# Optimization experiments

Measured on AMD Instinct MI355X. Metric: run time of the kernel, lower is better.

Reference implementation:

```python
import jax, jax.numpy as jnp
import numpy as np

MAX_RADIUS = 1.5
NUM_BASIS = 10
CS, CV = 16, 4              # scalar / vector multiplicities (input = query = key = output irreps)
DIM = CS + 3 * CV           # 28
SILU_GAIN = 1.679           # e3nn normalize2mom gain for silu


def _sus(x):
    # e3nn soft_unit_step: exp(-1/x) for x>0 else 0
    xp = jnp.where(x > 0, x, 1.0)
    return jnp.where(x > 0, jnp.exp(-1.0 / xp), 0.0)


def _fc(emb, w1, w2):
    # FullyConnectedNet([NUM_BASIS, 16, numel], act=silu), fan-in normalized
    h = SILU_GAIN * jax.nn.silu(emb @ w1 / jnp.sqrt(float(NUM_BASIS)))
    return h @ w2 / jnp.sqrt(16.0)


def _tp(fs, fv, sh1, w):
    # FullyConnectedTensorProduct((CS x0e + CV x1o) x (1x0e + 1x1o)) with per-edge weights w [...,400]
    # paths: 0e*0e->0e, 0e*1o->1o, 1o*0e->1o, 1o*1o->0e (sh l=0 component == 1)
    i0 = CS * CS; i1 = i0 + CS * CV; i2 = i1 + CV * CV
    lead = w.shape[:-1]
    w1 = w[..., :i0].reshape(lead + (CS, CS))
    w2 = w[..., i0:i1].reshape(lead + (CS, CV))
    w3 = w[..., i1:i2].reshape(lead + (CV, CV))
    w4 = w[..., i2:].reshape(lead + (CV, CS))
    out_s = (jnp.einsum('...c,...co->...o', fs, w1) / jnp.sqrt(float(CS))
             + jnp.einsum('...cx,...x,...co->...o', fv, sh1, w4) / jnp.sqrt(3.0 * CV)) / jnp.sqrt(2.0)
    out_v = (jnp.einsum('...c,...x,...co->...ox', fs, sh1, w2) / jnp.sqrt(float(CS))
             + jnp.einsum('...cx,...co->...ox', fv, w3) / jnp.sqrt(float(CV))) / jnp.sqrt(2.0)
    return out_s, out_v


def _forward(f, pos, wq_s, wq_v, fck_w1, fck_w2, fcv_w1, fcv_w2, dot_ws, dot_wv):
    B, N, _ = f.shape
    fs = f[..., :CS]                                    # [B,N,CS]
    fv = f[..., CS:].reshape(B, N, CV, 3)               # [B,N,CV,3]
    valid = jnp.any(f != 0, axis=-1)                    # mask of non-padded nodes

    # dense radius graph: i = dst, j = src; edge_vec = pos[src] - pos[dst]
    dvec = pos[:, None, :, :] - pos[:, :, None, :]      # [B,i,j,3]
    dist = jnp.sqrt(jnp.sum(dvec * dvec, axis=-1) + 1e-12)
    eye = jnp.eye(N, dtype=bool)
    mask = (dist < MAX_RADIUS) & (~eye)[None] & valid[:, :, None] & valid[:, None, :]
    sh1 = jnp.sqrt(3.0) * dvec / dist[..., None]        # component-normalized l=1 spherical harmonics

    # soft_one_hot_linspace, basis='smooth_finite', cutoff=True, scaled by sqrt(NB)
    step = MAX_RADIUS / (NUM_BASIS + 1)
    centers = jnp.linspace(0.0, MAX_RADIUS, NUM_BASIS + 2)[1:-1]
    diff = (dist[..., None] - centers) / step
    emb = (1.14136 * np.e ** 2) * _sus(diff + 1.0) * _sus(1.0 - diff)
    emb = emb * jnp.sqrt(float(NUM_BASIS))
    cutoff = _sus(10.0 * (1.0 - dist / MAX_RADIUS)) * mask

    # q = h_q(f): per-l linear
    q_s = fs @ wq_s / jnp.sqrt(float(CS))
    q_v = jnp.einsum('bncx,co->bnox', fv, wq_v) / jnp.sqrt(float(CV))

    wk = _fc(emb, fck_w1, fck_w2)                       # [B,N,N,400] per-edge TP weights
    wv = _fc(emb, fcv_w1, fcv_w2)
    k_s, k_v = _tp(fs[:, None], fv[:, None], sh1, wk)   # gather f[src] via broadcast over dst axis
    v_s, v_v = _tp(fs[:, None], fv[:, None], sh1, wv)

    # dot(q[dst], k) -> scalar per edge
    score = (jnp.einsum('bic,bijd,cd->bij', q_s, k_s, dot_ws) / jnp.sqrt(float(CS))
             + jnp.einsum('bicx,bijdx,cd->bij', q_v, k_v, dot_wv) / jnp.sqrt(3.0 * CV)) / jnp.sqrt(2.0)
    log_exp = cutoff * score
    z = jnp.sum(log_exp, axis=-1)                       # scatter-sum over src per dst node
    z = jnp.where(z == 0, 1.0, z)
    alpha = log_exp / z[:, :, None]
    r = jax.nn.relu(alpha)
    att = jnp.where(r > 0, jnp.sqrt(jnp.where(r > 0, r, 1.0)), 0.0)

    out_s = jnp.einsum('bij,bijo->bio', att, v_s)       # scatter-aggregate
    out_v = jnp.einsum('bij,bijox->biox', att, v_v)
    out = jnp.concatenate([out_s, out_v.reshape(B, N, 3 * CV)], axis=-1)
    return out * valid[..., None].astype(out.dtype)


def setup_inputs() -> dict:
    key = jax.random.key(0)
    ks = jax.random.split(key, 10)
    B, N = 4, 192
    NUMEL = CS * CS + CS * CV + CV * CV + CV * CS       # 400
    n = jax.random.normal
    return {
        'f': n(ks[0], (B, N, DIM), dtype=jnp.float32),
        'pos': 5.0 * jax.random.uniform(ks[1], (B, N, 3), dtype=jnp.float32),
        'wq_s': n(ks[2], (CS, CS), dtype=jnp.float32),
        'wq_v': n(ks[3], (CV, CV), dtype=jnp.float32),
        'fck_w1': n(ks[4], (NUM_BASIS, 16), dtype=jnp.float32),
        'fck_w2': n(ks[5], (16, NUMEL), dtype=jnp.float32),
        'fcv_w1': n(ks[6], (NUM_BASIS, 16), dtype=jnp.float32),
        'fcv_w2': n(ks[7], (16, NUMEL), dtype=jnp.float32),
        'dot_ws': n(ks[8], (CS, CS), dtype=jnp.float32),
        'dot_wv': n(ks[9], (CV, CV), dtype=jnp.float32),
    }


def reference(f, pos, wq_s, wq_v, fck_w1, fck_w2, fcv_w1, fcv_w2, dot_ws, dot_wv):
    return _forward(f, pos, wq_s, wq_v, fck_w1, fck_w2, fcv_w1, fcv_w2, dot_ws, dot_wv)
```

## Files before the change

kernel.cpp:

```cpp
#include <hip/hip_runtime.h>
#include <math.h>


#define NN 192
#define TSTRIDE 2560
#define MAXM 192

constexpr float C1   = 0.17677669529663687f;
constexpr float C2   = 0.17677669529663687f;
constexpr float C3   = 0.35355339059327373f;
constexpr float C4   = 0.20412414523193154f;
constexpr float CS1f = 0.17677669529663687f;
constexpr float CS2f = 0.20412414523193154f;
constexpr float RS10 = 0.31622776601683794f;
constexpr float GAIN4 = 1.679f * 0.25f;
constexpr float SQRT3 = 1.7320508075688772f;
constexpr float CEMB = (float)(1.14136 * 7.3890560989306495 * 3.1622776601683795);

__global__ __launch_bounds__(256) void precomp(
  const float* __restrict__ f, const float* __restrict__ wq_s, const float* __restrict__ wq_v,
  const float* __restrict__ w2k, const float* __restrict__ w2v,
  const float* __restrict__ dws, const float* __restrict__ dwv,
  float* __restrict__ T, float* __restrict__ qd, float* __restrict__ validf)
{
  const int node = blockIdx.x;
  const int tid  = threadIdx.x;
  __shared__ float Wsh[12800];
  __shared__ float fsh[28];
  __shared__ float qs_sh[16], qv_sh[12];
  __shared__ int vsh;
  if (tid == 0) vsh = 0;
  if (tid < 28) fsh[tid] = f[node*28 + tid];
  {
    float4* d = (float4*)Wsh;
    const float4* s0 = (const float4*)w2k;
    const float4* s1 = (const float4*)w2v;
    for (int q = tid; q < 1600; q += 256) { d[q] = s0[q]; d[1600 + q] = s1[q]; }
  }
  __syncthreads();
  if (tid < 28 && fsh[tid] != 0.f) vsh = 1;
  if (tid < 16) {
    float a = 0.f;
    #pragma unroll
    for (int c = 0; c < 16; ++c) a = fmaf(fsh[c], wq_s[c*16 + tid], a);
    qs_sh[tid] = a * 0.25f;
  } else if (tid < 28) {
    int idx = tid - 16, o = idx / 3, x = idx - o*3;
    float a = 0.f;
    #pragma unroll
    for (int c = 0; c < 4; ++c) a = fmaf(fsh[16 + c*3 + x], wq_v[c*4 + o], a);
    qv_sh[idx] = a * 0.5f;
  }
  __syncthreads();
  if (tid < 16) {
    float a = 0.f;
    #pragma unroll
    for (int c = 0; c < 16; ++c) a = fmaf(qs_sh[c], dws[c*16 + tid], a);
    qd[node*28 + tid] = a * CS1f;
  } else if (tid < 28) {
    int idx = tid - 16, d = idx / 3, x = idx - d*3;
    float a = 0.f;
    #pragma unroll
    for (int c = 0; c < 4; ++c) a = fmaf(qv_sh[c*3 + x], dwv[c*4 + d], a);
    qd[node*28 + tid] = a * CS2f;
  }
  if (tid == 0) validf[node] = vsh ? 1.f : 0.f;

  for (int e = tid; e < 2560; e += 256) {
    const int fc = e >= 1280 ? 1 : 0;
    const int r = e - fc*1280;
    const int h = r / 80, q = r - h*80;
    const float* W = Wsh + fc*6400 + h*400;
    float val = 0.f;
    if (q < 16) {
      #pragma unroll
      for (int c = 0; c < 16; ++c) val = fmaf(fsh[c], W[c*16 + q], val);
      val *= C1;
    } else if (q < 20) {
      const int o = q - 16;
      #pragma unroll
      for (int c = 0; c < 16; ++c) val = fmaf(fsh[c], W[256 + c*4 + o], val);
      val *= C2;
    } else if (q < 32) {
      const int p = q - 20, o = p / 3, x = p - o*3;
      #pragma unroll
      for (int c = 0; c < 4; ++c) val = fmaf(fsh[16 + c*3 + x], W[320 + c*4 + o], val);
      val *= C3;
    } else {
      const int p = q - 32, o = p / 3, x = p - o*3;
      #pragma unroll
      for (int c = 0; c < 4; ++c) val = fmaf(fsh[16 + c*3 + x], W[336 + c*16 + o], val);
      val *= C4;
    }
    T[(size_t)node*TSTRIDE + fc*1280 + (q >> 2)*64 + h*4 + (q & 3)] = val;
  }
}

__global__ __launch_bounds__(256) void se3_main(
  const float* __restrict__ pos, const float* __restrict__ w1k, const float* __restrict__ w1v,
  const float* __restrict__ T, const float* __restrict__ qd, const float* __restrict__ validf,
  float* __restrict__ out)
{
  const int bi = blockIdx.x;
  const int b = bi / NN, i = bi - b*NN;
  const int tid = threadIdx.x;
  const int lane = tid & 63, wid = tid >> 6;

  __shared__ float qd_sh[28];
  __shared__ float w1_sh[320];
  __shared__ int   s_node[MAXM];
  __shared__ float s_cut[MAXM], s_dist[MAXM];
  __shared__ float s_shx[MAXM], s_shy[MAXM], s_shz[MAXM];
  __shared__ float emb_sh[MAXM*10];
  __shared__ float Hk_sh[MAXM*16];
  __shared__ float Hv_sh[MAXM*16];
  __shared__ float le_sh[MAXM];
  __shared__ float att_sh[MAXM];
  __shared__ int   cnt_sh;
  __shared__ float red_sh[4];
  __shared__ float opart[4][28];

  if (tid < 28) qd_sh[tid] = qd[bi*28 + tid];
  if (tid < 160) {
    w1_sh[tid]       = w1k[tid] * RS10;
    w1_sh[160 + tid] = w1v[tid] * RS10;
  }
  if (tid == 0) cnt_sh = 0;
  const float pix = pos[bi*3+0], piy = pos[bi*3+1], piz = pos[bi*3+2];
  const float vali = validf[bi];
  __syncthreads();

  if (tid < NN) {
    const int nj = b*NN + tid;
    const float dx = pos[nj*3+0]-pix, dy = pos[nj*3+1]-piy, dz = pos[nj*3+2]-piz;
    const float dist = sqrtf(fmaf(dx,dx,fmaf(dy,dy,dz*dz)) + 1e-12f);
    if (tid != i && dist < 1.5f && vali != 0.f && validf[nj] != 0.f) {
      const float cut = expf(-1.f / (10.f * (1.f - dist * (1.f/1.5f))));
      if (cut > 0.f) {
        const int s = atomicAdd(&cnt_sh, 1);
        const float sc = SQRT3 / dist;
        s_node[s] = nj; s_cut[s] = cut; s_dist[s] = dist;
        s_shx[s] = dx*sc; s_shy[s] = dy*sc; s_shz[s] = dz*sc;
      }
    }
  }
  __syncthreads();
  const int M = cnt_sh;
  const int MK = M * 16;

  for (int idx = tid; idx < M*10; idx += 256) {
    const int pr = idx / 10, k = idx - pr*10;
    const float dd = (s_dist[pr] - (float)(k+1)*(1.5f/11.f)) * (11.f/1.5f);
    float e = 0.f;
    if (dd > -1.f && dd < 1.f) e = CEMB * expf(-1.f/(1.f+dd) - 1.f/(1.f-dd));
    emb_sh[idx] = e;
  }
  __syncthreads();

  for (int idx = tid; idx < M*32; idx += 256) {
    const int pr = idx >> 5, t = idx & 31, h = t & 15;
    const float* w = w1_sh + (t >> 4)*160;
    const float* e = emb_sh + pr*10;
    float s = 0.f;
    #pragma unroll
    for (int q = 0; q < 10; ++q) s = fmaf(e[q], w[q*16 + h], s);
    const float hh = GAIN4 * s / (1.f + expf(-s));
    float* dst = (t < 16) ? Hk_sh : Hv_sh;
    dst[pr*16 + h] = hh;
  }
  __syncthreads();

  for (int idx = tid; idx < MK; idx += 256) {
    const int pr = idx >> 4, h = idx & 15;
    const int node = s_node[pr];
    const float sx = s_shx[pr], sy = s_shy[pr], sz = s_shz[pr];
    const float a = Hk_sh[idx];
    const float4* b4 = (const float4*)(T + (size_t)node*TSTRIDE);
    float cc[80];
    float4* c4 = (float4*)cc;
    #pragma unroll
    for (int q = 0; q < 20; ++q) c4[q] = b4[q*16 + h];
    float s = 0.f;
    #pragma unroll
    for (int o = 0; o < 16; ++o) {
      const float t4 = fmaf(cc[32+3*o], sx, fmaf(cc[33+3*o], sy, cc[34+3*o]*sz));
      s = fmaf(qd_sh[o], cc[o] + t4, s);
    }
    #pragma unroll
    for (int o = 0; o < 4; ++o) {
      const float qvs = fmaf(qd_sh[16+3*o], sx, fmaf(qd_sh[17+3*o], sy, qd_sh[18+3*o]*sz));
      s = fmaf(qvs, cc[16+o], s);
      s = fmaf(qd_sh[16+3*o], cc[20+3*o+0], s);
      s = fmaf(qd_sh[17+3*o], cc[20+3*o+1], s);
      s = fmaf(qd_sh[18+3*o], cc[20+3*o+2], s);
    }
    s *= a;
    #pragma unroll
    for (int d = 1; d < 16; d <<= 1) s += __shfl_xor(s, d);
    if ((tid & 15) == 0) le_sh[pr] = s;
  }
  __syncthreads();

  float les = 0.f;
  if (tid < M) les = s_cut[tid] * le_sh[tid];
  float z = les;
  #pragma unroll
  for (int d = 1; d < 64; d <<= 1) z += __shfl_xor(z, d);
  if (lane == 0) red_sh[wid] = z;
  __syncthreads();
  z = red_sh[0] + red_sh[1] + red_sh[2] + red_sh[3];
  if (z == 0.f) z = 1.f;
  if (tid < M) {
    const float alpha = les / z;
    att_sh[tid] = alpha > 0.f ? sqrtf(alpha) : 0.f;
  }
  __syncthreads();

  float acc[28];
  #pragma unroll
  for (int c = 0; c < 28; ++c) acc[c] = 0.f;
  for (int idx = tid; idx < MK; idx += 256) {
    const int pr = idx >> 4, h = idx & 15;
    const int node = s_node[pr];
    const float sx = s_shx[pr], sy = s_shy[pr], sz = s_shz[pr];
    const float a = Hv_sh[idx] * att_sh[pr];
    const float4* b4 = (const float4*)(T + (size_t)node*TSTRIDE + 1280);
    float cc[80];
    float4* c4 = (float4*)cc;
    #pragma unroll
    for (int q = 0; q < 20; ++q) c4[q] = b4[q*16 + h];
    #pragma unroll
    for (int o = 0; o < 16; ++o) {
      const float t4 = fmaf(cc[32+3*o], sx, fmaf(cc[33+3*o], sy, cc[34+3*o]*sz));
      acc[o] = fmaf(a, cc[o] + t4, acc[o]);
    }
    const float ax = a*sx, ay = a*sy, az = a*sz;
    #pragma unroll
    for (int o = 0; o < 4; ++o) {
      const float t2 = cc[16+o];
      acc[16+3*o+0] = fmaf(ax, t2, fmaf(a, cc[20+3*o+0], acc[16+3*o+0]));
      acc[16+3*o+1] = fmaf(ay, t2, fmaf(a, cc[20+3*o+1], acc[16+3*o+1]));
      acc[16+3*o+2] = fmaf(az, t2, fmaf(a, cc[20+3*o+2], acc[16+3*o+2]));
    }
  }

  #pragma unroll
  for (int c = 0; c < 28; ++c) {
    float w = acc[c];
    #pragma unroll
    for (int d = 1; d < 64; d <<= 1) w += __shfl_xor(w, d);
    if (lane == 0) opart[wid][c] = w;
  }
  __syncthreads();
  if (tid < 28) out[bi*28 + tid] = opart[0][tid] + opart[1][tid] + opart[2][tid] + opart[3][tid];
}

extern "C" void kernel_launch(void* const* d_in, const int* in_sizes, int n_in,
                              void* d_out, int out_size, void* d_ws, size_t ws_size,
                              hipStream_t stream) {
  const float* f      = (const float*)d_in[0];
  const float* pos    = (const float*)d_in[1];
  const float* wq_s   = (const float*)d_in[2];
  const float* wq_v   = (const float*)d_in[3];
  const float* fck_w1 = (const float*)d_in[4];
  const float* fck_w2 = (const float*)d_in[5];
  const float* fcv_w1 = (const float*)d_in[6];
  const float* fcv_w2 = (const float*)d_in[7];
  const float* dot_ws = (const float*)d_in[8];
  const float* dot_wv = (const float*)d_in[9];
  float* outp = (float*)d_out;

  const int BN = in_sizes[0] / 28;

  float* T   = (float*)d_ws;
  float* qdp = T + (size_t)BN * TSTRIDE;
  float* vf  = qdp + (size_t)BN * 28;

  precomp<<<BN, 256, 0, stream>>>(f, wq_s, wq_v, fck_w2, fcv_w2, dot_ws, dot_wv, T, qdp, vf);
  se3_main<<<BN, 256, 0, stream>>>(pos, fck_w1, fcv_w1, T, qdp, vf, outp);
}
```

Measured before the change: 102.8 us.

## Fuse attention normalization into single pass using sign-split deferred sqrt accumulators

Merges the embedding, radial MLP, key-score, softmax-like normalization and value accumulation into one loop over neighbor×channel items. The attention weight sqrt(le/z) is rewritten as sqrt(le)/sqrt(z). Separate accumulators for positive and negative le are kept, and the sign of z picks one of them at the end. This removes several block barriers, the LDS staging arrays and a second pass over the neighbors. In exchange, each thread recomputes the radial basis and MLP for its item, and the doubled register accumulators raise register pressure.

After: 136.2 us. 1.32x slower.

```diff
diff --git a/kernel.cpp b/kernel.cpp
--- a/kernel.cpp
+++ b/kernel.cpp
@@ -111,14 +111,8 @@
   __shared__ int   s_node[MAXM];
   __shared__ float s_cut[MAXM], s_dist[MAXM];
   __shared__ float s_shx[MAXM], s_shy[MAXM], s_shz[MAXM];
-  __shared__ float emb_sh[MAXM*10];
-  __shared__ float Hk_sh[MAXM*16];
-  __shared__ float Hv_sh[MAXM*16];
-  __shared__ float le_sh[MAXM];
-  __shared__ float att_sh[MAXM];
   __shared__ int   cnt_sh;
-  __shared__ float red_sh[4];
-  __shared__ float opart[4][28];
+  __shared__ float opart[4][57];
 
   if (tid < 28) qd_sh[tid] = qd[bi*28 + tid];
   if (tid < 160) {
@@ -148,38 +142,40 @@
   const int M = cnt_sh;
   const int MK = M * 16;
 
-  for (int idx = tid; idx < M*10; idx += 256) {
-    const int pr = idx / 10, k = idx - pr*10;
-    const float dd = (s_dist[pr] - (float)(k+1)*(1.5f/11.f)) * (11.f/1.5f);
-    float e = 0.f;
-    if (dd > -1.f && dd < 1.f) e = CEMB * expf(-1.f/(1.f+dd) - 1.f/(1.f-dd));
-    emb_sh[idx] = e;
-  }
-  __syncthreads();
-
-  for (int idx = tid; idx < M*32; idx += 256) {
-    const int pr = idx >> 5, t = idx & 31, h = t & 15;
-    const float* w = w1_sh + (t >> 4)*160;
-    const float* e = emb_sh + pr*10;
-    float s = 0.f;
-    #pragma unroll
-    for (int q = 0; q < 10; ++q) s = fmaf(e[q], w[q*16 + h], s);
-    const float hh = GAIN4 * s / (1.f + expf(-s));
-    float* dst = (t < 16) ? Hk_sh : Hv_sh;
-    dst[pr*16 + h] = hh;
-  }
-  __syncthreads();
+  float accP[28], accN[28];
+  #pragma unroll
+  for (int c = 0; c < 28; ++c) { accP[c] = 0.f; accN[c] = 0.f; }
+  float zacc = 0.f;
 
   for (int idx = tid; idx < MK; idx += 256) {
     const int pr = idx >> 4, h = idx & 15;
     const int node = s_node[pr];
+    const float dist = s_dist[pr], cut = s_cut[pr];
     const float sx = s_shx[pr], sy = s_shy[pr], sz = s_shz[pr];
-    const float a = Hk_sh[idx];
-    const float4* b4 = (const float4*)(T + (size_t)node*TSTRIDE);
+
+    float emb[10];
+    #pragma unroll
+    for (int k = 0; k < 10; ++k) {
+      const float dd = (dist - (float)(k+1)*(1.5f/11.f)) * (11.f/1.5f);
+      float e = 0.f;
+      if (dd > -1.f && dd < 1.f) e = CEMB * expf(-1.f/(1.f+dd) - 1.f/(1.f-dd));
+      emb[k] = e;
+    }
+    float sk = 0.f, sv = 0.f;
+    #pragma unroll
+    for (int q = 0; q < 10; ++q) {
+      sk = fmaf(emb[q], w1_sh[q*16 + h], sk);
+      sv = fmaf(emb[q], w1_sh[160 + q*16 + h], sv);
+    }
+    const float Hk = GAIN4 * sk / (1.f + expf(-sk));
+    const float Hv = GAIN4 * sv / (1.f + expf(-sv));
+
+    const float4* __restrict__ bk = (const float4*)(T + (size_t)node*TSTRIDE);
     float cc[80];
     float4* c4 = (float4*)cc;
-    #pragma unroll
-    for (int q = 0; q < 20; ++q) c4[q] = b4[q*16 + h];
+
+    #pragma unroll
+    for (int q = 0; q < 20; ++q) c4[q] = bk[q*16 + h];
     float s = 0.f;
     #pragma unroll
     for (int o = 0; o < 16; ++o) {
@@ -194,65 +190,68 @@
       s = fmaf(qd_sh[17+3*o], cc[20+3*o+1], s);
       s = fmaf(qd_sh[18+3*o], cc[20+3*o+2], s);
     }
-    s *= a;
+    s *= Hk;
     #pragma unroll
     for (int d = 1; d < 16; d <<= 1) s += __shfl_xor(s, d);
-    if ((tid & 15) == 0) le_sh[pr] = s;
-  }
-  __syncthreads();
-
-  float les = 0.f;
-  if (tid < M) les = s_cut[tid] * le_sh[tid];
-  float z = les;
-  #pragma unroll
-  for (int d = 1; d < 64; d <<= 1) z += __shfl_xor(z, d);
-  if (lane == 0) red_sh[wid] = z;
-  __syncthreads();
-  z = red_sh[0] + red_sh[1] + red_sh[2] + red_sh[3];
-  if (z == 0.f) z = 1.f;
-  if (tid < M) {
-    const float alpha = les / z;
-    att_sh[tid] = alpha > 0.f ? sqrtf(alpha) : 0.f;
-  }
-  __syncthreads();
-
-  float acc[28];
-  #pragma unroll
-  for (int c = 0; c < 28; ++c) acc[c] = 0.f;
-  for (int idx = tid; idx < MK; idx += 256) {
-    const int pr = idx >> 4, h = idx & 15;
-    const int node = s_node[pr];
-    const float sx = s_shx[pr], sy = s_shy[pr], sz = s_shz[pr];
-    const float a = Hv_sh[idx] * att_sh[pr];
-    const float4* b4 = (const float4*)(T + (size_t)node*TSTRIDE + 1280);
-    float cc[80];
-    float4* c4 = (float4*)cc;
-    #pragma unroll
-    for (int q = 0; q < 20; ++q) c4[q] = b4[q*16 + h];
+    const float le = cut * s;
+    if (h == 0) zacc += le;
+    const float wp = sqrtf(fmaxf(le, 0.f));
+    const float wn = sqrtf(fmaxf(-le, 0.f));
+
+    const float4* __restrict__ bv = bk + 320;
+    #pragma unroll
+    for (int q = 0; q < 20; ++q) c4[q] = bv[q*16 + h];
     #pragma unroll
     for (int o = 0; o < 16; ++o) {
       const float t4 = fmaf(cc[32+3*o], sx, fmaf(cc[33+3*o], sy, cc[34+3*o]*sz));
-      acc[o] = fmaf(a, cc[o] + t4, acc[o]);
-    }
-    const float ax = a*sx, ay = a*sy, az = a*sz;
+      const float v = Hv * (cc[o] + t4);
+      accP[o] = fmaf(wp, v, accP[o]);
+      accN[o] = fmaf(wn, v, accN[o]);
+    }
     #pragma unroll
     for (int o = 0; o < 4; ++o) {
       const float t2 = cc[16+o];
-      acc[16+3*o+0] = fmaf(ax, t2, fmaf(a, cc[20+3*o+0], acc[16+3*o+0]));
-      acc[16+3*o+1] = fmaf(ay, t2, fmaf(a, cc[20+3*o+1], acc[16+3*o+1]));
-      acc[16+3*o+2] = fmaf(az, t2, fmaf(a, cc[20+3*o+2], acc[16+3*o+2]));
+      const float v0 = Hv * fmaf(sx, t2, cc[20+3*o+0]);
+      const float v1 = Hv * fmaf(sy, t2, cc[20+3*o+1]);
+      const float v2 = Hv * fmaf(sz, t2, cc[20+3*o+2]);
+      accP[16+3*o+0] = fmaf(wp, v0, accP[16+3*o+0]);
+      accP[16+3*o+1] = fmaf(wp, v1, accP[16+3*o+1]);
+      accP[16+3*o+2] = fmaf(wp, v2, accP[16+3*o+2]);
+      accN[16+3*o+0] = fmaf(wn, v0, accN[16+3*o+0]);
+      accN[16+3*o+1] = fmaf(wn, v1, accN[16+3*o+1]);
+      accN[16+3*o+2] = fmaf(wn, v2, accN[16+3*o+2]);
     }
   }
 
   #pragma unroll
   for (int c = 0; c < 28; ++c) {
-    float w = acc[c];
-    #pragma unroll
-    for (int d = 1; d < 64; d <<= 1) w += __shfl_xor(w, d);
-    if (lane == 0) opart[wid][c] = w;
-  }
-  __syncthreads();
-  if (tid < 28) out[bi*28 + tid] = opart[0][tid] + opart[1][tid] + opart[2][tid] + opart[3][tid];
+    float wv = accP[c];
+    #pragma unroll
+    for (int d = 1; d < 64; d <<= 1) wv += __shfl_xor(wv, d);
+    if (lane == 0) opart[wid][c] = wv;
+    float wn2 = accN[c];
+    #pragma unroll
+    for (int d = 1; d < 64; d <<= 1) wn2 += __shfl_xor(wn2, d);
+    if (lane == 0) opart[wid][28 + c] = wn2;
+  }
+  {
+    float zz = zacc;
+    #pragma unroll
+    for (int d = 1; d < 64; d <<= 1) zz += __shfl_xor(zz, d);
+    if (lane == 0) opart[wid][56] = zz;
+  }
+  __syncthreads();
+
+  if (tid < 28) {
+    const float z = opart[0][56] + opart[1][56] + opart[2][56] + opart[3][56];
+    const float aP = opart[0][tid] + opart[1][tid] + opart[2][tid] + opart[3][tid];
+    const float aN = opart[0][28+tid] + opart[1][28+tid] + opart[2][28+tid] + opart[3][28+tid];
+    float o;
+    if (z > 0.f)      o = aP / sqrtf(z);
+    else if (z < 0.f) o = aN / sqrtf(-z);
+    else              o = aP;
+    out[bi*28 + tid] = o;
+  }
 }
 
 extern "C" void kernel_launch(void* const* d_in, const int* in_sizes, int n_in,
```

## Fuse precompute into main kernel and contract key weights with query per block

Applied to the files above, without the earlier changes.

Removes the per-node precompute kernel that wrote a large per-node T table to global memory. The key path now folds the query vector into the key weights once per destination node (A/B/D/E tables in shared memory) and reads only the raw 28-float source features per edge. The value path applies the tensor product directly from shared fcv_w2 weights, and the radial MLP is computed inline instead of through a separate stage. This saves a launch and the global T round-trip, at the cost of loading w2v into shared memory in every block and doing more FMAs per edge in the value loop.

Measured after the change: 126.0 us. 22.6% more time.

```diff
diff --git a/kernel.cpp b/kernel.cpp
--- a/kernel.cpp
+++ b/kernel.cpp
@@ -3,8 +3,8 @@
 
 
 #define NN 192
-#define TSTRIDE 2560
 #define MAXM 192
+#define WVS 404
 
 constexpr float C1   = 0.17677669529663687f;
 constexpr float C2   = 0.17677669529663687f;
@@ -17,88 +17,12 @@
 constexpr float SQRT3 = 1.7320508075688772f;
 constexpr float CEMB = (float)(1.14136 * 7.3890560989306495 * 3.1622776601683795);
 
-__global__ __launch_bounds__(256) void precomp(
-  const float* __restrict__ f, const float* __restrict__ wq_s, const float* __restrict__ wq_v,
-  const float* __restrict__ w2k, const float* __restrict__ w2v,
+__global__ __launch_bounds__(256) void se3_fused(
+  const float* __restrict__ f, const float* __restrict__ pos,
+  const float* __restrict__ wq_s, const float* __restrict__ wq_v,
+  const float* __restrict__ w1k, const float* __restrict__ w2k,
+  const float* __restrict__ w1v, const float* __restrict__ w2v,
   const float* __restrict__ dws, const float* __restrict__ dwv,
-  float* __restrict__ T, float* __restrict__ qd, float* __restrict__ validf)
-{
-  const int node = blockIdx.x;
-  const int tid  = threadIdx.x;
-  __shared__ float Wsh[12800];
-  __shared__ float fsh[28];
-  __shared__ float qs_sh[16], qv_sh[12];
-  __shared__ int vsh;
-  if (tid == 0) vsh = 0;
-  if (tid < 28) fsh[tid] = f[node*28 + tid];
-  {
-    float4* d = (float4*)Wsh;
-    const float4* s0 = (const float4*)w2k;
-    const float4* s1 = (const float4*)w2v;
-    for (int q = tid; q < 1600; q += 256) { d[q] = s0[q]; d[1600 + q] = s1[q]; }
-  }
-  __syncthreads();
-  if (tid < 28 && fsh[tid] != 0.f) vsh = 1;
-  if (tid < 16) {
-    float a = 0.f;
-    #pragma unroll
-    for (int c = 0; c < 16; ++c) a = fmaf(fsh[c], wq_s[c*16 + tid], a);
-    qs_sh[tid] = a * 0.25f;
-  } else if (tid < 28) {
-    int idx = tid - 16, o = idx / 3, x = idx - o*3;
-    float a = 0.f;
-    #pragma unroll
-    for (int c = 0; c < 4; ++c) a = fmaf(fsh[16 + c*3 + x], wq_v[c*4 + o], a);
-    qv_sh[idx] = a * 0.5f;
-  }
-  __syncthreads();
-  if (tid < 16) {
-    float a = 0.f;
-    #pragma unroll
-    for (int c = 0; c < 16; ++c) a = fmaf(qs_sh[c], dws[c*16 + tid], a);
-    qd[node*28 + tid] = a * CS1f;
-  } else if (tid < 28) {
-    int idx = tid - 16, d = idx / 3, x = idx - d*3;
-    float a = 0.f;
-    #pragma unroll
-    for (int c = 0; c < 4; ++c) a = fmaf(qv_sh[c*3 + x], dwv[c*4 + d], a);
-    qd[node*28 + tid] = a * CS2f;
-  }
-  if (tid == 0) validf[node] = vsh ? 1.f : 0.f;
-
-  for (int e = tid; e < 2560; e += 256) {
-    const int fc = e >= 1280 ? 1 : 0;
-    const int r = e - fc*1280;
-    const int h = r / 80, q = r - h*80;
-    const float* W = Wsh + fc*6400 + h*400;
-    float val = 0.f;
-    if (q < 16) {
-      #pragma unroll
-      for (int c = 0; c < 16; ++c) val = fmaf(fsh[c], W[c*16 + q], val);
-      val *= C1;
-    } else if (q < 20) {
-      const int o = q - 16;
-      #pragma unroll
-      for (int c = 0; c < 16; ++c) val = fmaf(fsh[c], W[256 + c*4 + o], val);
-      val *= C2;
-    } else if (q < 32) {
-      const int p = q - 20, o = p / 3, x = p - o*3;
-      #pragma unroll
-      for (int c = 0; c < 4; ++c) val = fmaf(fsh[16 + c*3 + x], W[320 + c*4 + o], val);
-      val *= C3;
-    } else {
-      const int p = q - 32, o = p / 3, x = p - o*3;
-      #pragma unroll
-      for (int c = 0; c < 4; ++c) val = fmaf(fsh[16 + c*3 + x], W[336 + c*16 + o], val);
-      val *= C4;
-    }
-    T[(size_t)node*TSTRIDE + fc*1280 + (q >> 2)*64 + h*4 + (q & 3)] = val;
-  }
-}
-
-__global__ __launch_bounds__(256) void se3_main(
-  const float* __restrict__ pos, const float* __restrict__ w1k, const float* __restrict__ w1v,
-  const float* __restrict__ T, const float* __restrict__ qd, const float* __restrict__ validf,
   float* __restrict__ out)
 {
   const int bi = blockIdx.x;
@@ -106,41 +30,111 @@
   const int tid = threadIdx.x;
   const int lane = tid & 63, wid = tid >> 6;
 
+  __shared__ float Wv[16*WVS];
+  __shared__ float A_t[16][17];
+  __shared__ float B_t[16][4];
+  __shared__ float D_t[16][49];
+  __shared__ float E_t[16][13];
   __shared__ float qd_sh[28];
+  __shared__ float qs_sh[16], qv_sh[12];
+  __shared__ float fi_sh[28];
   __shared__ float w1_sh[320];
   __shared__ int   s_node[MAXM];
   __shared__ float s_cut[MAXM], s_dist[MAXM];
   __shared__ float s_shx[MAXM], s_shy[MAXM], s_shz[MAXM];
   __shared__ float emb_sh[MAXM*10];
-  __shared__ float Hk_sh[MAXM*16];
-  __shared__ float Hv_sh[MAXM*16];
-  __shared__ float le_sh[MAXM];
-  __shared__ float att_sh[MAXM];
-  __shared__ int   cnt_sh;
+  __shared__ float le_sh[MAXM], att_sh[MAXM];
+  __shared__ int   cnt_sh, vsh;
   __shared__ float red_sh[4];
   __shared__ float opart[4][28];
 
-  if (tid < 28) qd_sh[tid] = qd[bi*28 + tid];
-  if (tid < 160) {
-    w1_sh[tid]       = w1k[tid] * RS10;
-    w1_sh[160 + tid] = w1v[tid] * RS10;
-  }
-  if (tid == 0) cnt_sh = 0;
-  const float pix = pos[bi*3+0], piy = pos[bi*3+1], piz = pos[bi*3+2];
-  const float vali = validf[bi];
-  __syncthreads();
-
-  if (tid < NN) {
-    const int nj = b*NN + tid;
-    const float dx = pos[nj*3+0]-pix, dy = pos[nj*3+1]-piy, dz = pos[nj*3+2]-piz;
-    const float dist = sqrtf(fmaf(dx,dx,fmaf(dy,dy,dz*dz)) + 1e-12f);
-    if (tid != i && dist < 1.5f && vali != 0.f && validf[nj] != 0.f) {
-      const float cut = expf(-1.f / (10.f * (1.f - dist * (1.f/1.5f))));
-      if (cut > 0.f) {
-        const int s = atomicAdd(&cnt_sh, 1);
-        const float sc = SQRT3 / dist;
-        s_node[s] = nj; s_cut[s] = cut; s_dist[s] = dist;
-        s_shx[s] = dx*sc; s_shy[s] = dy*sc; s_shz[s] = dz*sc;
+  if (tid < 28) fi_sh[tid] = f[bi*28 + tid];
+  if (tid == 0) { cnt_sh = 0; vsh = 0; }
+  if (tid < 160) { w1_sh[tid] = w1k[tid]*RS10; w1_sh[160+tid] = w1v[tid]*RS10; }
+  for (int t = tid; t < 6400; t += 256) Wv[(t/400)*WVS + (t%400)] = w2v[t];
+  __syncthreads();
+
+  if (tid < 28 && fi_sh[tid] != 0.f) vsh = 1;
+  if (tid < 16) {
+    float a = 0.f;
+    #pragma unroll
+    for (int c = 0; c < 16; ++c) a = fmaf(fi_sh[c], wq_s[c*16 + tid], a);
+    qs_sh[tid] = a * 0.25f;
+  } else if (tid < 28) {
+    const int idx = tid - 16, o = idx / 3, x = idx - o*3;
+    float a = 0.f;
+    #pragma unroll
+    for (int c = 0; c < 4; ++c) a = fmaf(fi_sh[16 + c*3 + x], wq_v[c*4 + o], a);
+    qv_sh[idx] = a * 0.5f;
+  }
+  __syncthreads();
+  if (tid < 16) {
+    float a = 0.f;
+    #pragma unroll
+    for (int c = 0; c < 16; ++c) a = fmaf(qs_sh[c], dws[c*16 + tid], a);
+    qd_sh[tid] = a * CS1f;
+  } else if (tid < 28) {
+    const int idx = tid - 16, d2 = idx / 3, x = idx - d2*3;
+    float a = 0.f;
+    #pragma unroll
+    for (int c = 0; c < 4; ++c) a = fmaf(qv_sh[c*3 + x], dwv[c*4 + d2], a);
+    qd_sh[tid] = a * CS2f;
+  }
+  __syncthreads();
+  const int vali = vsh;
+
+  {
+    const int h = tid >> 4, c = tid & 15;
+    const float* Wr = w2k + h*400;
+    float a = 0.f;
+    #pragma unroll
+    for (int o = 0; o < 16; ++o) a = fmaf(qd_sh[o], Wr[c*16 + o], a);
+    A_t[h][c] = C1 * a;
+    #pragma unroll
+    for (int x = 0; x < 3; ++x) {
+      float d = 0.f;
+      #pragma unroll
+      for (int o = 0; o < 4; ++o) d = fmaf(qd_sh[16 + o*3 + x], Wr[256 + c*4 + o], d);
+      D_t[h][c*3 + x] = C2 * d;
+    }
+    if (c < 4) {
+      float bs = 0.f;
+      #pragma unroll
+      for (int o = 0; o < 16; ++o) bs = fmaf(qd_sh[o], Wr[336 + c*16 + o], bs);
+      B_t[h][c] = C4 * bs;
+      #pragma unroll
+      for (int x = 0; x < 3; ++x) {
+        float e = 0.f;
+        #pragma unroll
+        for (int o = 0; o < 4; ++o) e = fmaf(qd_sh[16 + o*3 + x], Wr[320 + c*4 + o], e);
+        E_t[h][c*3 + x] = C3 * e;
+      }
+    }
+  }
+
+  {
+    const float pix = pos[bi*3+0], piy = pos[bi*3+1], piz = pos[bi*3+2];
+    if (tid < NN) {
+      const int nj = b*NN + tid;
+      const float dx = pos[nj*3+0]-pix, dy = pos[nj*3+1]-piy, dz = pos[nj*3+2]-piz;
+      const float dist = sqrtf(fmaf(dx,dx,fmaf(dy,dy,dz*dz)) + 1e-12f);
+      if (tid != i && dist < 1.5f && vali) {
+        bool vj = false;
+        const float4* fj4 = (const float4*)(f + nj*28);
+        #pragma unroll
+        for (int q = 0; q < 7; ++q) {
+          const float4 v = fj4[q];
+          vj = vj || (v.x != 0.f) || (v.y != 0.f) || (v.z != 0.f) || (v.w != 0.f);
+        }
+        if (vj) {
+          const float cut = expf(-1.f / (10.f * (1.f - dist * (1.f/1.5f))));
+          if (cut > 0.f) {
+            const int s = atomicAdd(&cnt_sh, 1);
+            const float sc = SQRT3 / dist;
+            s_node[s] = nj; s_cut[s] = cut; s_dist[s] = dist;
+            s_shx[s] = dx*sc; s_shy[s] = dy*sc; s_shz[s] = dz*sc;
+          }
+        }
       }
     }
   }
@@ -157,44 +151,37 @@
   }
   __syncthreads();
 
-  for (int idx = tid; idx < M*32; idx += 256) {
-    const int pr = idx >> 5, t = idx & 31, h = t & 15;
-    const float* w = w1_sh + (t >> 4)*160;
-    const float* e = emb_sh + pr*10;
-    float s = 0.f;
-    #pragma unroll
-    for (int q = 0; q < 10; ++q) s = fmaf(e[q], w[q*16 + h], s);
-    const float hh = GAIN4 * s / (1.f + expf(-s));
-    float* dst = (t < 16) ? Hk_sh : Hv_sh;
-    dst[pr*16 + h] = hh;
-  }
-  __syncthreads();
-
   for (int idx = tid; idx < MK; idx += 256) {
     const int pr = idx >> 4, h = idx & 15;
     const int node = s_node[pr];
     const float sx = s_shx[pr], sy = s_shy[pr], sz = s_shz[pr];
-    const float a = Hk_sh[idx];
-    const float4* b4 = (const float4*)(T + (size_t)node*TSTRIDE);
-    float cc[80];
-    float4* c4 = (float4*)cc;
-    #pragma unroll
-    for (int q = 0; q < 20; ++q) c4[q] = b4[q*16 + h];
+    const float* e = emb_sh + pr*10;
+    float sk = 0.f;
+    #pragma unroll
+    for (int q = 0; q < 10; ++q) sk = fmaf(e[q], w1_sh[q*16 + h], sk);
+    const float Hk = GAIN4 * sk / (1.f + expf(-sk));
+
+    float fj[28];
+    {
+      const float4* fj4 = (const float4*)(f + node*28);
+      #pragma unroll
+      for (int q = 0; q < 7; ++q) ((float4*)fj)[q] = fj4[q];
+    }
     float s = 0.f;
     #pragma unroll
-    for (int o = 0; o < 16; ++o) {
-      const float t4 = fmaf(cc[32+3*o], sx, fmaf(cc[33+3*o], sy, cc[34+3*o]*sz));
-      s = fmaf(qd_sh[o], cc[o] + t4, s);
-    }
-    #pragma unroll
-    for (int o = 0; o < 4; ++o) {
-      const float qvs = fmaf(qd_sh[16+3*o], sx, fmaf(qd_sh[17+3*o], sy, qd_sh[18+3*o]*sz));
-      s = fmaf(qvs, cc[16+o], s);
-      s = fmaf(qd_sh[16+3*o], cc[20+3*o+0], s);
-      s = fmaf(qd_sh[17+3*o], cc[20+3*o+1], s);
-      s = fmaf(qd_sh[18+3*o], cc[20+3*o+2], s);
-    }
-    s *= a;
+    for (int c = 0; c < 16; ++c) {
+      const float t = A_t[h][c] + fmaf(sx, D_t[h][c*3], fmaf(sy, D_t[h][c*3+1], sz*D_t[h][c*3+2]));
+      s = fmaf(fj[c], t, s);
+    }
+    #pragma unroll
+    for (int c = 0; c < 4; ++c) {
+      const float g = fmaf(sx, fj[16+c*3], fmaf(sy, fj[17+c*3], sz*fj[18+c*3]));
+      s = fmaf(g, B_t[h][c], s);
+      s = fmaf(fj[16+c*3], E_t[h][c*3+0], s);
+      s = fmaf(fj[17+c*3], E_t[h][c*3+1], s);
+      s = fmaf(fj[18+c*3], E_t[h][c*3+2], s);
+    }
+    s *= Hk;
     #pragma unroll
     for (int d = 1; d < 16; d <<= 1) s += __shfl_xor(s, d);
     if ((tid & 15) == 0) le_sh[pr] = s;
@@ -223,24 +210,76 @@
     const int pr = idx >> 4, h = idx & 15;
     const int node = s_node[pr];
     const float sx = s_shx[pr], sy = s_shy[pr], sz = s_shz[pr];
-    const float a = Hv_sh[idx] * att_sh[pr];
-    const float4* b4 = (const float4*)(T + (size_t)node*TSTRIDE + 1280);
-    float cc[80];
-    float4* c4 = (float4*)cc;
-    #pragma unroll
-    for (int q = 0; q < 20; ++q) c4[q] = b4[q*16 + h];
-    #pragma unroll
-    for (int o = 0; o < 16; ++o) {
-      const float t4 = fmaf(cc[32+3*o], sx, fmaf(cc[33+3*o], sy, cc[34+3*o]*sz));
-      acc[o] = fmaf(a, cc[o] + t4, acc[o]);
-    }
-    const float ax = a*sx, ay = a*sy, az = a*sz;
-    #pragma unroll
-    for (int o = 0; o < 4; ++o) {
-      const float t2 = cc[16+o];
-      acc[16+3*o+0] = fmaf(ax, t2, fmaf(a, cc[20+3*o+0], acc[16+3*o+0]));
-      acc[16+3*o+1] = fmaf(ay, t2, fmaf(a, cc[20+3*o+1], acc[16+3*o+1]));
-      acc[16+3*o+2] = fmaf(az, t2, fmaf(a, cc[20+3*o+2], acc[16+3*o+2]));
+    const float* e = emb_sh + pr*10;
+    float sv = 0.f;
+    #pragma unroll
+    for (int q = 0; q < 10; ++q) sv = fmaf(e[q], w1_sh[160 + q*16 + h], sv);
+    const float Hv = GAIN4 * sv / (1.f + expf(-sv));
+    const float a = Hv * att_sh[pr];
+
+    float fj[28];
+    {
+      const float4* fj4 = (const float4*)(f + node*28);
+      #pragma unroll
+      for (int q = 0; q < 7; ++q) ((float4*)fj)[q] = fj4[q];
+    }
+    const float* Wr = Wv + h*WVS;
+
+    const float aC1 = a * C1;
+    #pragma unroll
+    for (int c = 0; c < 16; ++c) {
+      const float m = aC1 * fj[c];
+      const float4* w = (const float4*)(Wr + c*16);
+      const float4 w0 = w[0], w1 = w[1], w2 = w[2], w3 = w[3];
+      acc[0]  = fmaf(m, w0.x, acc[0]);  acc[1]  = fmaf(m, w0.y, acc[1]);
+      acc[2]  = fmaf(m, w0.z, acc[2]);  acc[3]  = fmaf(m, w0.w, acc[3]);
+      acc[4]  = fmaf(m, w1.x, acc[4]);  acc[5]  = fmaf(m, w1.y, acc[5]);
+      acc[6]  = fmaf(m, w1.z, acc[6]);  acc[7]  = fmaf(m, w1.w, acc[7]);
+      acc[8]  = fmaf(m, w2.x, acc[8]);  acc[9]  = fmaf(m, w2.y, acc[9]);
+      acc[10] = fmaf(m, w2.z, acc[10]); acc[11] = fmaf(m, w2.w, acc[11]);
+      acc[12] = fmaf(m, w3.x, acc[12]); acc[13] = fmaf(m, w3.y, acc[13]);
+      acc[14] = fmaf(m, w3.z, acc[14]); acc[15] = fmaf(m, w3.w, acc[15]);
+    }
+    const float aC4 = a * C4;
+    #pragma unroll
+    for (int c = 0; c < 4; ++c) {
+      const float g = fmaf(sx, fj[16+c*3], fmaf(sy, fj[17+c*3], sz*fj[18+c*3]));
+      const float m = aC4 * g;
+      const float4* w = (const float4*)(Wr + 336 + c*16);
+      const float4 w0 = w[0], w1 = w[1], w2 = w[2], w3 = w[3];
+      acc[0]  = fmaf(m, w0.x, acc[0]);  acc[1]  = fmaf(m, w0.y, acc[1]);
+      acc[2]  = fmaf(m, w0.z, acc[2]);  acc[3]  = fmaf(m, w0.w, acc[3]);
+      acc[4]  = fmaf(m, w1.x, acc[4]);  acc[5]  = fmaf(m, w1.y, acc[5]);
+      acc[6]  = fmaf(m, w1.z, acc[6]);  acc[7]  = fmaf(m, w1.w, acc[7]);
+      acc[8]  = fmaf(m, w2.x, acc[8]);  acc[9]  = fmaf(m, w2.y, acc[9]);
+      acc[10] = fmaf(m, w2.z, acc[10]); acc[11] = fmaf(m, w2.w, acc[11]);
+      acc[12] = fmaf(m, w3.x, acc[12]); acc[13] = fmaf(m, w3.y, acc[13]);
+      acc[14] = fmaf(m, w3.z, acc[14]); acc[15] = fmaf(m, w3.w, acc[15]);
+    }
+    float t0 = 0.f, t1 = 0.f, t2 = 0.f, t3 = 0.f;
+    #pragma unroll
+    for (int c = 0; c < 16; ++c) {
+      const float4 w = *(const float4*)(Wr + 256 + c*4);
+      t0 = fmaf(fj[c], w.x, t0); t1 = fmaf(fj[c], w.y, t1);
+      t2 = fmaf(fj[c], w.z, t2); t3 = fmaf(fj[c], w.w, t3);
+    }
+    const float aC2 = a * C2;
+    {
+      const float u0 = aC2*t0, u1 = aC2*t1, u2 = aC2*t2, u3 = aC2*t3;
+      acc[16] = fmaf(sx, u0, acc[16]); acc[17] = fmaf(sy, u0, acc[17]); acc[18] = fmaf(sz, u0, acc[18]);
+      acc[19] = fmaf(sx, u1, acc[19]); acc[20] = fmaf(sy, u1, acc[20]); acc[21] = fmaf(sz, u1, acc[21]);
+      acc[22] = fmaf(sx, u2, acc[22]); acc[23] = fmaf(sy, u2, acc[23]); acc[24] = fmaf(sz, u2, acc[24]);
+      acc[25] = fmaf(sx, u3, acc[25]); acc[26] = fmaf(sy, u3, acc[26]); acc[27] = fmaf(sz, u3, acc[27]);
+    }
+    const float aC3 = a * C3;
+    #pragma unroll
+    for (int c = 0; c < 4; ++c) {
+      const float4 w = *(const float4*)(Wr + 320 + c*4);
+      const float vx = aC3*fj[16+c*3], vy = aC3*fj[17+c*3], vz = aC3*fj[18+c*3];
+      acc[16] = fmaf(vx, w.x, acc[16]); acc[17] = fmaf(vy, w.x, acc[17]); acc[18] = fmaf(vz, w.x, acc[18]);
+      acc[19] = fmaf(vx, w.y, acc[19]); acc[20] = fmaf(vy, w.y, acc[20]); acc[21] = fmaf(vz, w.y, acc[21]);
+      acc[22] = fmaf(vx, w.z, acc[22]); acc[23] = fmaf(vy, w.z, acc[23]); acc[24] = fmaf(vz, w.z, acc[24]);
+      acc[25] = fmaf(vx, w.w, acc[25]); acc[26] = fmaf(vy, w.w, acc[26]); acc[27] = fmaf(vz, w.w, acc[27]);
     }
   }
 
@@ -272,10 +311,7 @@
 
   const int BN = in_sizes[0] / 28;
 
-  float* T   = (float*)d_ws;
-  float* qdp = T + (size_t)BN * TSTRIDE;
-  float* vf  = qdp + (size_t)BN * 28;
-
-  precomp<<<BN, 256, 0, stream>>>(f, wq_s, wq_v, fck_w2, fcv_w2, dot_ws, dot_wv, T, qdp, vf);
-  se3_main<<<BN, 256, 0, stream>>>(pos, fck_w1, fcv_w1, T, qdp, vf, outp);
+  se3_fused<<<BN, 256, 0, stream>>>(f, pos, wq_s, wq_v,
+                                    fck_w1, fck_w2, fcv_w1, fcv_w2,
+                                    dot_ws, dot_wv, outp);
 }
```
